# Optimization experiments

Measured on AMD Instinct MI355X. Metric: run time of the kernel, lower is better.

The kernel has to match this reference:

```python
import jax, jax.numpy as jnp
import numpy as np

D_INP = 3584
D_HIDE = 65536
BATCH = 2048
TOP_K = 7


def setup_inputs() -> dict:
    key = jax.random.key(0)
    kx, kw = jax.random.split(key)
    x = jax.random.normal(kx, (BATCH, D_INP), dtype=jnp.float32)
    # kaiming-uniform-ish init, scaled so pre-activations are O(1)
    bound = float(np.sqrt(6.0 / D_INP))
    W_enc = jax.random.uniform(kw, (D_INP, D_HIDE), dtype=jnp.float32,
                               minval=-bound, maxval=bound)
    b_enc = jnp.zeros((D_HIDE,), dtype=jnp.float32)
    b_dec = jnp.zeros((D_INP,), dtype=jnp.float32)
    return {"x": x, "W_enc": W_enc, "b_enc": b_enc, "b_dec": b_dec, "top_k": TOP_K}


def _mask_topk(h: jnp.ndarray, k: int) -> jnp.ndarray:
    # binary mask keeping only top-k values per row (scatter of ones at top-k idx)
    _, idx = jax.lax.top_k(h, k)                 # (B, k)
    rows = jnp.arange(h.shape[0])[:, None]       # (B, 1)
    return jnp.zeros_like(h).at[rows, idx].set(1.0)


def reference(x, W_enc, b_enc, b_dec, top_k):
    # encode: dense GEMM + top-k mask + relu
    h = (x - b_dec) @ W_enc + b_enc              # (B, d_hide)
    features = jax.nn.relu(h * _mask_topk(h, top_k))
    reconstructed = features @ W_enc.T + b_dec   # (B, d_inp)
    return (reconstructed, features)
```

## Files before the change

### kernel.cpp

```cpp
#include <hip/hip_runtime.h>
#include <hip/hip_bf16.h>
#include <hip/hip_fp8.h>
#include <stdint.h>

#define D_INP  3584
#define D_HIDE 65536
#define BATCH  2048
#define TOPK   7
#define MARGIN1 0.5f
#define MARGIN2 0.03f
#define TFIX   3.8f
#define SPILL_CAP 768
#define CAND_CAP 160
#define T2_CAP 32

typedef __attribute__((ext_vector_type(8)))  short s16x8;
typedef __attribute__((ext_vector_type(4)))  float f32x4;
typedef __attribute__((ext_vector_type(16))) float f32x16;
typedef __attribute__((ext_vector_type(4)))  int   v4i;
typedef __attribute__((ext_vector_type(8)))  int   v8i;

#define AS1 __attribute__((address_space(1)))
#define AS3 __attribute__((address_space(3)))

__device__ __forceinline__ void gload_lds16(const void* g, void* l) {
    __builtin_amdgcn_global_load_lds((const AS1 void*)g, (AS3 void*)l, 16, 0, 0);
}

__device__ __forceinline__ float bf16_bits_to_f32(unsigned short u) {
    union { unsigned int i; float f; } c;
    c.i = ((unsigned int)u) << 16;
    return c.f;
}
__device__ __forceinline__ float f16_bits_to_f32(unsigned short u) {
    _Float16 h;
    __builtin_memcpy(&h, &u, 2);
    return (float)h;
}
__device__ __forceinline__ unsigned short f32_to_f16_bits(float f) {
    _Float16 h = (_Float16)f;
    unsigned short u;
    __builtin_memcpy(&u, &h, 2);
    return u;
}

__device__ __forceinline__ unsigned int pack4_fp8(float a, float b, float c, float d) {
#if __has_builtin(__builtin_amdgcn_cvt_pk_fp8_f32)
    int lo = __builtin_amdgcn_cvt_pk_fp8_f32(a, b, 0, false);
    int w  = __builtin_amdgcn_cvt_pk_fp8_f32(c, d, lo, true);
    return (unsigned int)w;
#else
    auto one = [](float f) -> unsigned int {
        __hip_fp8_e4m3 q(f);
        return (unsigned int)q.__x;
    };
    return one(a) | (one(b) << 8) | (one(c) << 16) | (one(d) << 24);
#endif
}

__global__ __launch_bounds__(256) void build_a_kernel(
    const float* __restrict__ x, const float* __restrict__ b_dec,
    unsigned char* __restrict__ A) {
    const int n8 = BATCH * D_INP / 8;
    const int stride = gridDim.x * blockDim.x;
    for (int i = blockIdx.x * blockDim.x + threadIdx.x; i < n8; i += stride) {
        int c8 = i % (D_INP / 8);
        float4 x0 = ((const float4*)x)[i * 2];
        float4 x1 = ((const float4*)x)[i * 2 + 1];
        float4 b0 = ((const float4*)b_dec)[c8 * 2];
        float4 b1 = ((const float4*)b_dec)[c8 * 2 + 1];
        uint2 w;
        w.x = pack4_fp8(x0.x - b0.x, x0.y - b0.y, x0.z - b0.z, x0.w - b0.w);
        w.y = pack4_fp8(x1.x - b1.x, x1.y - b1.y, x1.z - b1.z, x1.w - b1.w);
        ((uint2*)A)[i] = w;
    }
}

__global__ __launch_bounds__(256) void transpose_w_kernel(
    const float* __restrict__ W, unsigned char* __restrict__ Wq,
    __hip_bfloat16* __restrict__ Whi, unsigned short* __restrict__ Wlo) {
    __shared__ float tile[64][68];
    const int tid = threadIdx.x;
    const int n0 = blockIdx.x * 64;
    const int k0 = blockIdx.y * 64;

    const int lk  = tid >> 4;
    const int ln4 = (tid & 15) * 4;
    #pragma unroll
    for (int p = 0; p < 4; ++p) {
        float4 v = *(const float4*)&W[(size_t)(k0 + p * 16 + lk) * D_HIDE + n0 + ln4];
        *(float4*)&tile[p * 16 + lk][ln4] = v;
    }
    __syncthreads();

    const int sn  = tid >> 4;
    const int sk4 = (tid & 15) * 4;
    #pragma unroll
    for (int p = 0; p < 4; ++p) {
        int n_loc = p * 16 + sn;
        float v[4];
        #pragma unroll
        for (int j = 0; j < 4; ++j) v[j] = tile[sk4 + j][n_loc];
        size_t o = (size_t)(n0 + n_loc) * D_INP + k0 + sk4;
        ushort4 hi4, lo4;
        #pragma unroll
        for (int j = 0; j < 4; ++j) {
            __hip_bfloat16 hb = __float2bfloat16(v[j]);
            unsigned short hbits;
            __builtin_memcpy(&hbits, &hb, 2);
            ((unsigned short*)&hi4)[j] = hbits;
            float fv = __bfloat162float(hb);
            ((unsigned short*)&lo4)[j] = f32_to_f16_bits((v[j] - fv) * 4096.0f);
        }
        *(ushort4*)((unsigned short*)Whi + o) = hi4;
        *(ushort4*)(Wlo + o) = lo4;
        *(unsigned int*)(Wq + o) =
            pack4_fp8(v[0] * 128.0f, v[1] * 128.0f, v[2] * 128.0f, v[3] * 128.0f);
    }
}

#define GBM 128
#define GBN 128
#define GBK 64
#define NKT (D_INP / GBK)
#define SLOT8 8192

__global__ __launch_bounds__(256, 3) void gemm_enc_kernel(
    const unsigned char* __restrict__ A,
    const unsigned char* __restrict__ Bq,
    const float* __restrict__ b_enc,
    int2* __restrict__ Spill, int* __restrict__ SpillCnt) {
    __shared__ char lds[49152];
    char* Asl = lds;
    char* Bsl = lds + 3 * SLOT8;

    const int bid = blockIdx.x;
    const int g = (bid & 7) * 1024 + (bid >> 3);
    const int mt = g & 15;
    const int nt = g >> 4;

    const int tid  = threadIdx.x;
    const int lane = tid & 63;
    const int wave = tid >> 6;
    const int wm = wave >> 1;
    const int wn = wave & 1;
    const int l31 = lane & 31;
    const int l5  = lane >> 5;

    const unsigned char* Abase = A  + (size_t)(mt * GBM) * D_INP;
    const unsigned char* Bbase = Bq + (size_t)(nt * GBN) * D_INP;

    const int srow = lane >> 2;
    const int sunit = (lane & 3) ^ ((lane >> 3) & 3);
    const size_t gsrc0 = (size_t)((wave * 2 + 0) * 16 + srow) * D_INP + sunit * 16;
    const size_t gsrc1 = (size_t)((wave * 2 + 1) * 16 + srow) * D_INP + sunit * 16;
    const int ldst0 = (wave * 2 + 0) * 1024;
    const int ldst1 = (wave * 2 + 1) * 1024;

    int offALo[2], offAHi[2], offBLo[2], offBHi[2];
    const int uA = l5 * 2;
    #pragma unroll
    for (int mi = 0; mi < 2; ++mi) {
        int r = wm * 64 + mi * 32 + l31;
        int s = (r >> 1) & 3;
        offALo[mi] = r * 64 + ((uA ^ s) & 3) * 16;
        offAHi[mi] = r * 64 + (((uA + 1) ^ s) & 3) * 16;
    }
    #pragma unroll
    for (int ni = 0; ni < 2; ++ni) {
        int r = wn * 64 + ni * 32 + l31;
        int s = (r >> 1) & 3;
        offBLo[ni] = r * 64 + ((uA ^ s) & 3) * 16;
        offBHi[ni] = r * 64 + (((uA + 1) ^ s) & 3) * 16;
    }

#define STAGE(t_, sA_, sB_)                                                    \
    {                                                                          \
        size_t ko_ = (size_t)(t_) * GBK;                                       \
        gload_lds16(Abase + gsrc0 + ko_, (sA_) + ldst0);                       \
        gload_lds16(Abase + gsrc1 + ko_, (sA_) + ldst1);                       \
        gload_lds16(Bbase + gsrc0 + ko_, (sB_) + ldst0);                       \
        gload_lds16(Bbase + gsrc1 + ko_, (sB_) + ldst1);                       \
    }
#define LDFRAG(dst, base_, offLo_, offHi_)                                     \
    {                                                                          \
        v4i lo_ = *(const v4i*)((base_) + (offLo_));                           \
        v4i hi_ = *(const v4i*)((base_) + (offHi_));                           \
        dst = __builtin_shufflevector(lo_, hi_, 0, 1, 2, 3, 4, 5, 6, 7);       \
    }

    f32x16 acc[2][2];
    #pragma unroll
    for (int mi = 0; mi < 2; ++mi)
        #pragma unroll
        for (int ni = 0; ni < 2; ++ni)
            #pragma unroll
            for (int q = 0; q < 16; ++q) acc[mi][ni][q] = 0.f;

    STAGE(0, Asl + 0 * SLOT8, Bsl + 0 * SLOT8)
    STAGE(1, Asl + 1 * SLOT8, Bsl + 1 * SLOT8)
    asm volatile("s_waitcnt vmcnt(4)" ::: "memory");
    __builtin_amdgcn_s_barrier();
    __builtin_amdgcn_sched_barrier(0);

    const int SA = 0x7F7F7F7F;
    const int SB = 0x78787878;

    int sl = 0;
    #pragma unroll 1
    for (int t = 0; t < NKT; ++t) {
        const char* As = Asl + sl * SLOT8;
        const char* Bs = Bsl + sl * SLOT8;
        int sl2 = sl + 2; if (sl2 >= 3) sl2 -= 3;
        int st = t + 2; if (st >= NKT) st -= NKT;

        v8i aF[2], bF[2];
        LDFRAG(aF[0], As, offALo[0], offAHi[0])
        LDFRAG(aF[1], As, offALo[1], offAHi[1])
        LDFRAG(bF[0], Bs, offBLo[0], offBHi[0])
        LDFRAG(bF[1], Bs, offBLo[1], offBHi[1])
        STAGE(st, Asl + sl2 * SLOT8, Bsl + sl2 * SLOT8)
        acc[0][0] = __builtin_amdgcn_mfma_scale_f32_32x32x64_f8f6f4(
            aF[0], bF[0], acc[0][0], 0, 0, 0, SA, 0, SB);
        acc[0][1] = __builtin_amdgcn_mfma_scale_f32_32x32x64_f8f6f4(
            aF[0], bF[1], acc[0][1], 0, 0, 0, SA, 0, SB);
        acc[1][0] = __builtin_amdgcn_mfma_scale_f32_32x32x64_f8f6f4(
            aF[1], bF[0], acc[1][0], 0, 0, 0, SA, 0, SB);
        acc[1][1] = __builtin_amdgcn_mfma_scale_f32_32x32x64_f8f6f4(
            aF[1], bF[1], acc[1][1], 0, 0, 0, SA, 0, SB);
        asm volatile("s_waitcnt vmcnt(4)" ::: "memory");
        __builtin_amdgcn_s_barrier();
        __builtin_amdgcn_sched_barrier(0);

        sl = sl + 1; if (sl >= 3) sl -= 3;
    }
#undef STAGE
#undef LDFRAG

    const int orow0 = mt * GBM + wm * 64;
    const int ocol0 = nt * GBN + wn * 64;
    float be[2];
    #pragma unroll
    for (int ni = 0; ni < 2; ++ni) be[ni] = b_enc[ocol0 + ni * 32 + l31];
    #pragma unroll
    for (int mi = 0; mi < 2; ++mi) {
        #pragma unroll
        for (int ni = 0; ni < 2; ++ni) {
            #pragma unroll
            for (int q = 0; q < 16; ++q) {
                float v = acc[mi][ni][q] + be[ni];
                if (v >= TFIX) {
                    int grow = orow0 + mi * 32 + (q & 3) + 8 * (q >> 2) + 4 * l5;
                    int col  = ocol0 + ni * 32 + l31;
                    int qq = atomicAdd(&SpillCnt[grow], 1);
                    if (qq < SPILL_CAP)
                        Spill[(size_t)grow * SPILL_CAP + qq] =
                            make_int2(__float_as_int(v), col);
                }
            }
        }
    }
}

__global__ __launch_bounds__(256) void merge_full_kernel(
    const int2* __restrict__ Spill, const int* __restrict__ SpillCnt,
    const float* __restrict__ x, const float* __restrict__ b_dec,
    const float* __restrict__ b_enc,
    const __hip_bfloat16* __restrict__ Whi, const unsigned short* __restrict__ Wlo,
    float* __restrict__ out0, float* __restrict__ feat) {
    const int row = blockIdx.x;
    const int tid = threadIdx.x;

    __shared__ float xs[D_INP];
    __shared__ float ev[SPILL_CAP];
    __shared__ int   ec[SPILL_CAP];
    __shared__ float rv[256];
    __shared__ int   ri[256];
    __shared__ int   scnt, t2cnt;
    __shared__ int   cidx[CAND_CAP];
    __shared__ float cval[CAND_CAP];
    __shared__ int   c2col[T2_CAP];
    __shared__ double c2val[T2_CAP];
    __shared__ int   fidx[TOPK];
    __shared__ float fval[TOPK];

    for (int i = tid; i < D_INP / 4; i += 256) {
        float4 xv = ((const float4*)(x + (size_t)row * D_INP))[i];
        float4 bd = ((const float4*)b_dec)[i];
        float4 r;
        r.x = xv.x - bd.x; r.y = xv.y - bd.y;
        r.z = xv.z - bd.z; r.w = xv.w - bd.w;
        ((float4*)xs)[i] = r;
    }
    int cnt = SpillCnt[row];
    if (cnt > SPILL_CAP) cnt = SPILL_CAP;
    for (int i = tid; i < cnt; i += 256) {
        int2 e = Spill[(size_t)row * SPILL_CAP + i];
        ev[i] = __int_as_float(e.x);
        ec[i] = e.y;
    }
    if (tid == 0) { scnt = 0; t2cnt = 0; }
    __syncthreads();

    float lv[3] = {-1e30f, -1e30f, -1e30f};
    #pragma unroll
    for (int k = 0; k < 3; ++k) {
        int i = tid + k * 256;
        if (i < cnt) {
            float v = ev[i];
            if (v > lv[2]) {
                lv[2] = v;
                if (lv[2] > lv[1]) { float t = lv[2]; lv[2] = lv[1]; lv[1] = t; }
                if (lv[1] > lv[0]) { float t = lv[1]; lv[1] = lv[0]; lv[0] = t; }
            }
        }
    }
    float t7s = -1e30f;
    for (int it = 0; it < TOPK; ++it) {
        rv[tid] = lv[0];
        ri[tid] = tid;
        __syncthreads();
        for (int s = 128; s > 0; s >>= 1) {
            if (tid < s && rv[tid + s] > rv[tid]) {
                rv[tid] = rv[tid + s]; ri[tid] = ri[tid + s];
            }
            __syncthreads();
        }
        t7s = rv[0];
        int w = ri[0];
        __syncthreads();
        if (tid == w) { lv[0] = lv[1]; lv[1] = lv[2]; lv[2] = -1e30f; }
    }

    const float T1 = t7s - MARGIN1;
    #pragma unroll
    for (int k = 0; k < 3; ++k) {
        int i = tid + k * 256;
        if (i < cnt && ev[i] >= T1) {
            int q = atomicAdd(&scnt, 1);
            if (q < CAND_CAP) cidx[q] = ec[i];
        }
    }
    __syncthreads();
    const int ncand = scnt < CAND_CAP ? scnt : CAND_CAP;

    const int lane = tid & 63, wv = tid >> 6;
    for (int c = wv; c < ncand; c += 4) {
        int col = cidx[c];
        const s16x8* hi8p = (const s16x8*)(Whi + (size_t)col * D_INP);
        float sh = 0.f;
        for (int k = lane; k < D_INP / 8; k += 64) {
            s16x8 h8 = hi8p[k];
            #pragma unroll
            for (int j = 0; j < 8; ++j)
                sh = fmaf(xs[k * 8 + j], bf16_bits_to_f32((unsigned short)h8[j]), sh);
        }
        #pragma unroll
        for (int off = 32; off > 0; off >>= 1) sh += __shfl_down(sh, off);
        if (lane == 0) cval[c] = sh + b_enc[col];
    }
    __syncthreads();

    rv[tid] = (tid < ncand) ? cval[tid] : -1e30f;
    __syncthreads();
    float t7h = -1e30f;
    for (int it = 0; it < TOPK; ++it) {
        __shared__ float pv[256]; __shared__ int pi[256];
        pv[tid] = rv[tid]; pi[tid] = tid;
        __syncthreads();
        for (int s = 128; s > 0; s >>= 1) {
            if (tid < s && pv[tid + s] > pv[tid]) {
                pv[tid] = pv[tid + s]; pi[tid] = pi[tid + s];
            }
            __syncthreads();
        }
        t7h = pv[0];
        int w = pi[0];
        __syncthreads();
        if (tid == w) rv[tid] = -1e30f;
        __syncthreads();
    }

    const float T2 = t7h - MARGIN2;
    if (tid < ncand && cval[tid] >= T2) {
        int q = atomicAdd(&t2cnt, 1);
        if (q < T2_CAP) c2col[q] = cidx[tid];
    }
    __syncthreads();
    const int nt2 = t2cnt < T2_CAP ? t2cnt : T2_CAP;

    for (int c = wv; c < nt2; c += 4) {
        int col = c2col[c];
        const s16x8* hi8p = (const s16x8*)(Whi + (size_t)col * D_INP);
        const s16x8* lo8p = (const s16x8*)(Wlo + (size_t)col * D_INP);
        double s = 0.0;
        for (int k = lane; k < D_INP / 8; k += 64) {
            s16x8 h8 = hi8p[k];
            s16x8 l8 = lo8p[k];
            #pragma unroll
            for (int j = 0; j < 8; ++j) {
                double w = (double)bf16_bits_to_f32((unsigned short)h8[j])
                         + (double)f16_bits_to_f32((unsigned short)l8[j]) * (1.0 / 4096.0);
                s += (double)xs[k * 8 + j] * w;
            }
        }
        #pragma unroll
        for (int off = 32; off > 0; off >>= 1) s += __shfl_down(s, off);
        if (lane == 0) c2val[c] = s + (double)b_enc[col];
    }
    __syncthreads();

    if (tid == 0) {
        for (int t = 0; t < TOPK; ++t) {
            double bestv = -1e30; int bestc = -1;
            for (int c = 0; c < nt2; ++c) {
                double v = c2val[c];
                if (v > bestv || (v == bestv && bestc >= 0 && c2col[c] < c2col[bestc])) {
                    bestv = v; bestc = c;
                }
            }
            if (bestc >= 0) {
                fidx[t] = c2col[bestc];
                fval[t] = bestv > 0.0 ? (float)bestv : 0.f;
                c2val[bestc] = -1e30;
            } else { fidx[t] = 0; fval[t] = 0.f; }
        }
    }
    __syncthreads();

    float* frow = feat + (size_t)row * D_HIDE;
    float4 z4 = make_float4(0.f, 0.f, 0.f, 0.f);
    for (int i = tid; i < D_HIDE / 4; i += 256) ((float4*)frow)[i] = z4;
    __syncthreads();
    if (tid < TOPK) frow[fidx[tid]] = fval[tid];

    float* orow = out0 + (size_t)row * D_INP;
    for (int i = tid; i < D_INP / 8; i += 256) {
        float a[8];
        float4 b0 = ((const float4*)b_dec)[i * 2];
        float4 b1 = ((const float4*)b_dec)[i * 2 + 1];
        a[0] = b0.x; a[1] = b0.y; a[2] = b0.z; a[3] = b0.w;
        a[4] = b1.x; a[5] = b1.y; a[6] = b1.z; a[7] = b1.w;
        #pragma unroll
        for (int t = 0; t < TOPK; ++t) {
            s16x8 h8 = *(const s16x8*)(Whi + (size_t)fidx[t] * D_INP + i * 8);
            float vt = fval[t];
            #pragma unroll
            for (int j = 0; j < 8; ++j)
                a[j] = fmaf(vt, bf16_bits_to_f32((unsigned short)h8[j]), a[j]);
        }
        float4 o0 = make_float4(a[0], a[1], a[2], a[3]);
        float4 o1 = make_float4(a[4], a[5], a[6], a[7]);
        ((float4*)(orow + i * 8))[0] = o0;
        ((float4*)(orow + i * 8))[1] = o1;
    }
}

extern "C" void kernel_launch(void* const* d_in, const int* in_sizes, int n_in,
                              void* d_out, int out_size, void* d_ws, size_t ws_size,
                              hipStream_t stream) {
    const float* x     = (const float*)d_in[0];
    const float* W     = (const float*)d_in[1];
    const float* b_enc = (const float*)d_in[2];
    const float* b_dec = (const float*)d_in[3];

    float* out0 = (float*)d_out;
    float* feat = (float*)d_out + (size_t)BATCH * D_INP;

    uint8_t* ws = (uint8_t*)d_ws;
    unsigned char* Wq = ws;
    size_t off = (size_t)D_HIDE * D_INP;
    __hip_bfloat16* Whi = (__hip_bfloat16*)(ws + off);
    off += (size_t)D_HIDE * D_INP * 2;
    unsigned short* Wlo = (unsigned short*)(ws + off);
    off += (size_t)D_HIDE * D_INP * 2;
    unsigned char* A = ws + off;
    off += (size_t)BATCH * D_INP;
    int2* Spill = (int2*)(ws + off);
    off += (size_t)BATCH * SPILL_CAP * 8;
    int* SpillCnt = (int*)(ws + off);
    off += (size_t)BATCH * 4;

    hipMemsetAsync(SpillCnt, 0, BATCH * sizeof(int), stream);
    hipLaunchKernelGGL(build_a_kernel, dim3(2048), dim3(256), 0, stream,
                       x, b_dec, A);
    hipLaunchKernelGGL(transpose_w_kernel, dim3(D_HIDE / 64, D_INP / 64), dim3(256), 0, stream,
                       W, Wq, Whi, Wlo);
    hipLaunchKernelGGL(gemm_enc_kernel, dim3((BATCH / GBM) * (D_HIDE / GBN)), dim3(256), 0, stream,
                       A, Wq, b_enc, Spill, SpillCnt);
    hipLaunchKernelGGL(merge_full_kernel, dim3(BATCH), dim3(256), 0, stream,
                       Spill, SpillCnt, x, b_dec, b_enc, Whi, Wlo, out0, feat);
}
```

Measured before the change: 1.385 ms.

## Switch FP8 encoder GEMM to 16x16x128 MFMA with K=128 double-buffered tiles

Rewrites the main FP8 encoder GEMM loop to use 16x16x128 scaled MFMAs, keeping a 4x4 accumulator grid per wave. Each K step now covers 128 bytes, giving 28 iterations with two-stage double buffering in 64KB LDS instead of triple-buffered 64-byte steps. The block-to-tile mapping is also reordered to group neighbouring M/N tiles. The aim is fewer loop iterations and barriers and more MFMA work per LDS fragment load. In exchange, occupancy drops to 2 blocks per CU and the wait now drains all outstanding loads (vmcnt(0)) every iteration, which reduces load/compute overlap.

Measured after the change: 1.406 ms. Within noise of the previous version (+1.5%).

```diff
diff --git a/kernel.cpp b/kernel.cpp
--- a/kernel.cpp
+++ b/kernel.cpp
@@ -16,7 +16,6 @@
 
 typedef __attribute__((ext_vector_type(8)))  short s16x8;
 typedef __attribute__((ext_vector_type(4)))  float f32x4;
-typedef __attribute__((ext_vector_type(16))) float f32x16;
 typedef __attribute__((ext_vector_type(4)))  int   v4i;
 typedef __attribute__((ext_vector_type(8)))  int   v8i;
 
@@ -121,137 +120,129 @@
 
 #define GBM 128
 #define GBN 128
-#define GBK 64
-#define NKT (D_INP / GBK)
-#define SLOT8 8192
-
-__global__ __launch_bounds__(256, 3) void gemm_enc_kernel(
+#define NKT 28
+
+__global__ __launch_bounds__(256, 2) void gemm_enc_kernel(
     const unsigned char* __restrict__ A,
     const unsigned char* __restrict__ Bq,
     const float* __restrict__ b_enc,
     int2* __restrict__ Spill, int* __restrict__ SpillCnt) {
-    __shared__ char lds[49152];
-    char* Asl = lds;
-    char* Bsl = lds + 3 * SLOT8;
+    __shared__ char lds[65536];
+    char* Ab = lds;
+    char* Bb = lds + 32768;
 
     const int bid = blockIdx.x;
-    const int g = (bid & 7) * 1024 + (bid >> 3);
-    const int mt = g & 15;
-    const int nt = g >> 4;
+    const int x = bid & 7;
+    const int j = bid >> 3;
+    const int mt = (j & 7) | ((x & 1) << 3);
+    const int nt = (j >> 3) | ((x >> 1) << 7);
 
     const int tid  = threadIdx.x;
     const int lane = tid & 63;
     const int wave = tid >> 6;
     const int wm = wave >> 1;
     const int wn = wave & 1;
-    const int l31 = lane & 31;
-    const int l5  = lane >> 5;
+    const int fr = lane & 15;
+    const int fg = lane >> 4;
 
     const unsigned char* Abase = A  + (size_t)(mt * GBM) * D_INP;
     const unsigned char* Bbase = Bq + (size_t)(nt * GBN) * D_INP;
 
     const int srow = lane >> 2;
-    const int sunit = (lane & 3) ^ ((lane >> 3) & 3);
-    const size_t gsrc0 = (size_t)((wave * 2 + 0) * 16 + srow) * D_INP + sunit * 16;
-    const size_t gsrc1 = (size_t)((wave * 2 + 1) * 16 + srow) * D_INP + sunit * 16;
-    const int ldst0 = (wave * 2 + 0) * 1024;
-    const int ldst1 = (wave * 2 + 1) * 1024;
-
-    int offALo[2], offAHi[2], offBLo[2], offBHi[2];
-    const int uA = l5 * 2;
-    #pragma unroll
-    for (int mi = 0; mi < 2; ++mi) {
-        int r = wm * 64 + mi * 32 + l31;
-        int s = (r >> 1) & 3;
-        offALo[mi] = r * 64 + ((uA ^ s) & 3) * 16;
-        offAHi[mi] = r * 64 + (((uA + 1) ^ s) & 3) * 16;
-    }
-    #pragma unroll
-    for (int ni = 0; ni < 2; ++ni) {
-        int r = wn * 64 + ni * 32 + l31;
-        int s = (r >> 1) & 3;
-        offBLo[ni] = r * 64 + ((uA ^ s) & 3) * 16;
-        offBHi[ni] = r * 64 + (((uA + 1) ^ s) & 3) * 16;
-    }
-
-#define STAGE(t_, sA_, sB_)                                                    \
+    const int usel = (lane & 3) ^ ((lane >> 3) & 3);
+    const size_t g0 = (size_t)((wave * 2 + 0) * 16 + srow) * D_INP + usel * 32;
+    const size_t g1 = (size_t)((wave * 2 + 1) * 16 + srow) * D_INP + usel * 32;
+    const int l0 = (wave * 2 + 0) * 1024;
+    const int l1 = (wave * 2 + 1) * 1024;
+
+    int offA[4], offB[4];
+    const int s = (fr >> 1) & 3;
+    #pragma unroll
+    for (int m = 0; m < 4; ++m) {
+        int rA = wm * 64 + m * 16 + fr;
+        offA[m] = rA * 64 + ((fg ^ s) & 3) * 16;
+        int rB = wn * 64 + m * 16 + fr;
+        offB[m] = rB * 64 + ((fg ^ s) & 3) * 16;
+    }
+
+#define STAGE(d_, t_)                                                          \
     {                                                                          \
-        size_t ko_ = (size_t)(t_) * GBK;                                       \
-        gload_lds16(Abase + gsrc0 + ko_, (sA_) + ldst0);                       \
-        gload_lds16(Abase + gsrc1 + ko_, (sA_) + ldst1);                       \
-        gload_lds16(Bbase + gsrc0 + ko_, (sB_) + ldst0);                       \
-        gload_lds16(Bbase + gsrc1 + ko_, (sB_) + ldst1);                       \
-    }
-#define LDFRAG(dst, base_, offLo_, offHi_)                                     \
+        size_t ko_ = (size_t)(t_) * 128;                                       \
+        char* al_ = Ab + (d_) * 16384;                                         \
+        char* bl_ = Bb + (d_) * 16384;                                         \
+        gload_lds16(Abase + g0 + ko_,      al_ + l0);                          \
+        gload_lds16(Abase + g0 + ko_ + 16, al_ + 8192 + l0);                   \
+        gload_lds16(Abase + g1 + ko_,      al_ + l1);                          \
+        gload_lds16(Abase + g1 + ko_ + 16, al_ + 8192 + l1);                   \
+        gload_lds16(Bbase + g0 + ko_,      bl_ + l0);                          \
+        gload_lds16(Bbase + g0 + ko_ + 16, bl_ + 8192 + l0);                   \
+        gload_lds16(Bbase + g1 + ko_,      bl_ + l1);                          \
+        gload_lds16(Bbase + g1 + ko_ + 16, bl_ + 8192 + l1);                   \
+    }
+#define LDFRAG(dst, sub_, off_)                                                \
     {                                                                          \
-        v4i lo_ = *(const v4i*)((base_) + (offLo_));                           \
-        v4i hi_ = *(const v4i*)((base_) + (offHi_));                           \
+        v4i lo_ = *(const v4i*)((sub_) + (off_));                              \
+        v4i hi_ = *(const v4i*)((sub_) + 8192 + (off_));                       \
         dst = __builtin_shufflevector(lo_, hi_, 0, 1, 2, 3, 4, 5, 6, 7);       \
     }
 
-    f32x16 acc[2][2];
-    #pragma unroll
-    for (int mi = 0; mi < 2; ++mi)
-        #pragma unroll
-        for (int ni = 0; ni < 2; ++ni)
-            #pragma unroll
-            for (int q = 0; q < 16; ++q) acc[mi][ni][q] = 0.f;
-
-    STAGE(0, Asl + 0 * SLOT8, Bsl + 0 * SLOT8)
-    STAGE(1, Asl + 1 * SLOT8, Bsl + 1 * SLOT8)
-    asm volatile("s_waitcnt vmcnt(4)" ::: "memory");
+    f32x4 acc[4][4];
+    #pragma unroll
+    for (int m = 0; m < 4; ++m)
+        #pragma unroll
+        for (int n = 0; n < 4; ++n) acc[m][n] = (f32x4){0.f, 0.f, 0.f, 0.f};
+
+    STAGE(0, 0)
+    asm volatile("s_waitcnt vmcnt(0)" ::: "memory");
     __builtin_amdgcn_s_barrier();
     __builtin_amdgcn_sched_barrier(0);
 
     const int SA = 0x7F7F7F7F;
     const int SB = 0x78787878;
 
-    int sl = 0;
     #pragma unroll 1
     for (int t = 0; t < NKT; ++t) {
-        const char* As = Asl + sl * SLOT8;
-        const char* Bs = Bsl + sl * SLOT8;
-        int sl2 = sl + 2; if (sl2 >= 3) sl2 -= 3;
-        int st = t + 2; if (st >= NKT) st -= NKT;
-
-        v8i aF[2], bF[2];
-        LDFRAG(aF[0], As, offALo[0], offAHi[0])
-        LDFRAG(aF[1], As, offALo[1], offAHi[1])
-        LDFRAG(bF[0], Bs, offBLo[0], offBHi[0])
-        LDFRAG(bF[1], Bs, offBLo[1], offBHi[1])
-        STAGE(st, Asl + sl2 * SLOT8, Bsl + sl2 * SLOT8)
-        acc[0][0] = __builtin_amdgcn_mfma_scale_f32_32x32x64_f8f6f4(
-            aF[0], bF[0], acc[0][0], 0, 0, 0, SA, 0, SB);
-        acc[0][1] = __builtin_amdgcn_mfma_scale_f32_32x32x64_f8f6f4(
-            aF[0], bF[1], acc[0][1], 0, 0, 0, SA, 0, SB);
-        acc[1][0] = __builtin_amdgcn_mfma_scale_f32_32x32x64_f8f6f4(
-            aF[1], bF[0], acc[1][0], 0, 0, 0, SA, 0, SB);
-        acc[1][1] = __builtin_amdgcn_mfma_scale_f32_32x32x64_f8f6f4(
-            aF[1], bF[1], acc[1][1], 0, 0, 0, SA, 0, SB);
-        asm volatile("s_waitcnt vmcnt(4)" ::: "memory");
+        const int d = t & 1;
+        int st = t + 1; if (st >= NKT) st -= NKT;
+        STAGE(d ^ 1, st)
+
+        const char* As = Ab + d * 16384;
+        const char* Bs = Bb + d * 16384;
+        v8i aF[4], bF[4];
+        #pragma unroll
+        for (int m = 0; m < 4; ++m) LDFRAG(aF[m], As, offA[m])
+        #pragma unroll
+        for (int n = 0; n < 4; ++n) LDFRAG(bF[n], Bs, offB[n])
+
+        #pragma unroll
+        for (int m = 0; m < 4; ++m)
+            #pragma unroll
+            for (int n = 0; n < 4; ++n)
+                acc[m][n] = __builtin_amdgcn_mfma_scale_f32_16x16x128_f8f6f4(
+                    aF[m], bF[n], acc[m][n], 0, 0, 0, SA, 0, SB);
+
+        asm volatile("s_waitcnt vmcnt(0)" ::: "memory");
         __builtin_amdgcn_s_barrier();
         __builtin_amdgcn_sched_barrier(0);
-
-        sl = sl + 1; if (sl >= 3) sl -= 3;
     }
 #undef STAGE
 #undef LDFRAG
 
     const int orow0 = mt * GBM + wm * 64;
     const int ocol0 = nt * GBN + wn * 64;
-    float be[2];
-    #pragma unroll
-    for (int ni = 0; ni < 2; ++ni) be[ni] = b_enc[ocol0 + ni * 32 + l31];
-    #pragma unroll
-    for (int mi = 0; mi < 2; ++mi) {
-        #pragma unroll
-        for (int ni = 0; ni < 2; ++ni) {
+    float be[4];
+    #pragma unroll
+    for (int n = 0; n < 4; ++n) be[n] = b_enc[ocol0 + n * 16 + fr];
+    #pragma unroll
+    for (int m = 0; m < 4; ++m) {
+        #pragma unroll
+        for (int n = 0; n < 4; ++n) {
             #pragma unroll
-            for (int q = 0; q < 16; ++q) {
-                float v = acc[mi][ni][q] + be[ni];
+            for (int q = 0; q < 4; ++q) {
+                float v = acc[m][n][q] + be[n];
                 if (v >= TFIX) {
-                    int grow = orow0 + mi * 32 + (q & 3) + 8 * (q >> 2) + 4 * l5;
-                    int col  = ocol0 + ni * 32 + l31;
+                    int grow = orow0 + m * 16 + fg * 4 + q;
+                    int col  = ocol0 + n * 16 + fr;
                     int qq = atomicAdd(&SpillCnt[grow], 1);
                     if (qq < SPILL_CAP)
                         Spill[(size_t)grow * SPILL_CAP + qq] =
@@ -320,9 +311,9 @@
         rv[tid] = lv[0];
         ri[tid] = tid;
         __syncthreads();
-        for (int s = 128; s > 0; s >>= 1) {
-            if (tid < s && rv[tid + s] > rv[tid]) {
-                rv[tid] = rv[tid + s]; ri[tid] = ri[tid + s];
+        for (int ss = 128; ss > 0; ss >>= 1) {
+            if (tid < ss && rv[tid + ss] > rv[tid]) {
+                rv[tid] = rv[tid + ss]; ri[tid] = ri[tid + ss];
             }
             __syncthreads();
         }
@@ -352,8 +343,8 @@
         for (int k = lane; k < D_INP / 8; k += 64) {
             s16x8 h8 = hi8p[k];
             #pragma unroll
-            for (int j = 0; j < 8; ++j)
-                sh = fmaf(xs[k * 8 + j], bf16_bits_to_f32((unsigned short)h8[j]), sh);
+            for (int jj = 0; jj < 8; ++jj)
+                sh = fmaf(xs[k * 8 + jj], bf16_bits_to_f32((unsigned short)h8[jj]), sh);
         }
         #pragma unroll
         for (int off = 32; off > 0; off >>= 1) sh += __shfl_down(sh, off);
@@ -368,9 +359,9 @@
         __shared__ float pv[256]; __shared__ int pi[256];
         pv[tid] = rv[tid]; pi[tid] = tid;
         __syncthreads();
-        for (int s = 128; s > 0; s >>= 1) {
-            if (tid < s && pv[tid + s] > pv[tid]) {
-                pv[tid] = pv[tid + s]; pi[tid] = pi[tid + s];
+        for (int ss = 128; ss > 0; ss >>= 1) {
+            if (tid < ss && pv[tid + ss] > pv[tid]) {
+                pv[tid] = pv[tid + ss]; pi[tid] = pi[tid + ss];
             }
             __syncthreads();
         }
@@ -393,20 +384,20 @@
         int col = c2col[c];
         const s16x8* hi8p = (const s16x8*)(Whi + (size_t)col * D_INP);
         const s16x8* lo8p = (const s16x8*)(Wlo + (size_t)col * D_INP);
-        double s = 0.0;
+        double sd = 0.0;
         for (int k = lane; k < D_INP / 8; k += 64) {
             s16x8 h8 = hi8p[k];
             s16x8 l8 = lo8p[k];
             #pragma unroll
-            for (int j = 0; j < 8; ++j) {
-                double w = (double)bf16_bits_to_f32((unsigned short)h8[j])
-                         + (double)f16_bits_to_f32((unsigned short)l8[j]) * (1.0 / 4096.0);
-                s += (double)xs[k * 8 + j] * w;
-            }
-        }
-        #pragma unroll
-        for (int off = 32; off > 0; off >>= 1) s += __shfl_down(s, off);
-        if (lane == 0) c2val[c] = s + (double)b_enc[col];
+            for (int jj = 0; jj < 8; ++jj) {
+                double w = (double)bf16_bits_to_f32((unsigned short)h8[jj])
+                         + (double)f16_bits_to_f32((unsigned short)l8[jj]) * (1.0 / 4096.0);
+                sd += (double)xs[k * 8 + jj] * w;
+            }
+        }
+        #pragma unroll
+        for (int off = 32; off > 0; off >>= 1) sd += __shfl_down(sd, off);
+        if (lane == 0) c2val[c] = sd + (double)b_enc[col];
     }
     __syncthreads();
 
@@ -446,8 +437,8 @@
             s16x8 h8 = *(const s16x8*)(Whi + (size_t)fidx[t] * D_INP + i * 8);
             float vt = fval[t];
             #pragma unroll
-            for (int j = 0; j < 8; ++j)
-                a[j] = fmaf(vt, bf16_bits_to_f32((unsigned short)h8[j]), a[j]);
+            for (int jj = 0; jj < 8; ++jj)
+                a[jj] = fmaf(vt, bf16_bits_to_f32((unsigned short)h8[jj]), a[jj]);
         }
         float4 o0 = make_float4(a[0], a[1], a[2], a[3]);
         float4 o1 = make_float4(a[4], a[5], a[6], a[7]);
```
